# Optimization experiments

Measured on AMD Instinct MI355X. Metric: run time of the kernel, lower is better.

## Reference

```python
import jax, jax.numpy as jnp
import numpy as np

T, N, F, E, P, G, H, B = 8, 40000, 256, 640000, 128, 128, 128, 1024

def setup_inputs() -> dict:
    key = jax.random.key(0)
    ks = jax.random.split(key, 20)
    s = 0.05
    inp = {
        "x": jax.random.normal(ks[0], (T, N, F), jnp.float32),
        "edge_index": jax.random.randint(ks[1], (2, E), 0, N, dtype=jnp.int64),
        "target_indices": jax.random.randint(ks[2], (B,), 0, N, dtype=jnp.int64),
        # projection layer
        "proj_w": jax.random.normal(ks[3], (F, P), jnp.float32) * s,
        "proj_b": jnp.zeros((P,), jnp.float32),
        # GCN layers (weight + bias, symmetric-norm GCNConv with self-loops)
        "gcn_w1": jax.random.normal(ks[4], (P, G), jnp.float32) * s,
        "gcn_b1": jnp.zeros((G,), jnp.float32),
        "gcn_w2": jax.random.normal(ks[5], (G, G), jnp.float32) * s,
        "gcn_b2": jnp.zeros((G,), jnp.float32),
        # GRU (PyTorch layout: [3H, in], gates order r,z,n)
        "gru_w_ih": jax.random.normal(ks[6], (3 * H, 2 * G), jnp.float32) * s,
        "gru_w_hh": jax.random.normal(ks[7], (3 * H, H), jnp.float32) * s,
        "gru_b_ih": jnp.zeros((3 * H,), jnp.float32),
        "gru_b_hh": jnp.zeros((3 * H,), jnp.float32),
        # attention pooling
        "attn_w": jax.random.normal(ks[8], (H, 1), jnp.float32) * s,
        "attn_b": jnp.zeros((1,), jnp.float32),
        # predictor MLP (dropout in eval mode -> identity)
        "pred_w1": jax.random.normal(ks[9], (H, 16), jnp.float32) * s,
        "pred_b1": jnp.zeros((16,), jnp.float32),
        "pred_w2": jax.random.normal(ks[10], (16, 1), jnp.float32) * s,
        "pred_b2": jnp.zeros((1,), jnp.float32),
    }
    return inp


def reference(x, edge_index, target_indices, proj_w, proj_b, gcn_w1, gcn_b1,
              gcn_w2, gcn_b2, gru_w_ih, gru_w_hh, gru_b_ih, gru_b_hh,
              attn_w, attn_b, pred_w1, pred_b1, pred_w2, pred_b2):
    n = x.shape[1]
    # GCNConv normalization: add self-loops, deg^-1/2 A_hat deg^-1/2
    loops = jnp.arange(n, dtype=edge_index.dtype)
    src = jnp.concatenate([edge_index[0], loops])
    dst = jnp.concatenate([edge_index[1], loops])
    deg = jax.ops.segment_sum(jnp.ones_like(src, x.dtype), dst, num_segments=n)
    dinv = jnp.where(deg > 0, jax.lax.rsqrt(deg), 0.0)
    norm = (dinv[src] * dinv[dst])[:, None]  # [E+N, 1]

    def gcn_layer(h, w, b):
        m = h @ w                               # [N, G]
        agg = jax.ops.segment_sum(m[src] * norm, dst, num_segments=n)
        return jax.nn.relu(agg + b)

    def per_step(xt):
        h = jax.nn.relu(xt @ proj_w + proj_b)    # projection
        h1 = gcn_layer(h, gcn_w1, gcn_b1)
        h2 = gcn_layer(h1, gcn_w2, gcn_b2)
        return jnp.concatenate([h1, h2], axis=-1)  # jumping-knowledge concat

    emb = jax.vmap(per_step)(x)                  # [T, N, 2G]
    tgt = emb[:, target_indices]                 # [T, B, 2G]

    hdim = gru_w_hh.shape[1]
    def gru_cell(h, xt):
        gi = xt @ gru_w_ih.T + gru_b_ih
        gh = h @ gru_w_hh.T + gru_b_hh
        ir, iz, ig = jnp.split(gi, 3, axis=-1)
        hr, hz, hg = jnp.split(gh, 3, axis=-1)
        r = jax.nn.sigmoid(ir + hr)
        z = jax.nn.sigmoid(iz + hz)
        g = jnp.tanh(ig + r * hg)
        h_new = (1.0 - z) * g + z * h
        return h_new, h_new

    h0 = jnp.zeros((tgt.shape[1], hdim), x.dtype)
    _, outs = jax.lax.scan(gru_cell, h0, tgt)    # [T, B, H]
    rnn_out = outs.transpose(1, 0, 2)            # [B, T, H]

    scores = jnp.tanh(rnn_out @ attn_w + attn_b)       # [B, T, 1]
    attn_weights = jax.nn.softmax(scores, axis=1)
    rep = jnp.sum(rnn_out * attn_weights, axis=1)      # [B, H]

    hmid = jax.nn.relu(rep @ pred_w1 + pred_b1)        # dropout: eval mode
    pred = hmid @ pred_w2 + pred_b2                    # [B, 1]
    return pred, attn_weights.squeeze(-1)
```

## Files before the change

### kernel.cpp

```cpp
#include <hip/hip_runtime.h>
#include <stdint.h>

#define TT 8
#define NN 40000
#define FF 256
#define EE 640000
#define BB 1024
#define ROWS 320000

typedef __attribute__((ext_vector_type(8))) short s16x8;
typedef __attribute__((ext_vector_type(4))) float f32x4;

__device__ __forceinline__ unsigned short f2bf(float f){
  unsigned int u = __float_as_uint(f);
  u += 0x7fffu + ((u >> 16) & 1u);
  return (unsigned short)(u >> 16);
}
__device__ __forceinline__ float bflo(unsigned int u){ return __uint_as_float(u << 16); }
__device__ __forceinline__ float bfhi(unsigned int u){ return __uint_as_float(u & 0xffff0000u); }

__device__ __forceinline__ void gl2lds16(const void* g, void* l){
  auto gp = reinterpret_cast<const unsigned int __attribute__((address_space(1)))*>(
      reinterpret_cast<uintptr_t>(g));
  auto lp = reinterpret_cast<unsigned int __attribute__((address_space(3)))*>(
      static_cast<unsigned int>(reinterpret_cast<uintptr_t>(l)));
  __builtin_amdgcn_global_load_lds(gp, lp, 16, 0, 0);
}

__global__ void prep_k(const float* __restrict__ proj_w, const float* __restrict__ w1,
                       const float* __restrict__ w2, const float* __restrict__ wih,
                       const float* __restrict__ whh,
                       unsigned short* __restrict__ projwt, unsigned short* __restrict__ w1t,
                       unsigned short* __restrict__ w2t, unsigned short* __restrict__ wihb,
                       uint2* __restrict__ whhp)
{
  int i = blockIdx.x * 256 + threadIdx.x;
  if (i < 32768) {
    int p = i >> 8, f = i & 255;
    projwt[i] = f2bf(proj_w[f * 128 + p]);
  } else if (i < 49152) {
    int k = i - 32768; int o = k >> 7, c = k & 127;
    w1t[k] = f2bf(w1[c * 128 + o]);
  } else if (i < 65536) {
    int k = i - 49152; int o = k >> 7, c = k & 127;
    w2t[k] = f2bf(w2[c * 128 + o]);
  } else if (i < 163840) {
    int k = i - 65536;
    wihb[k] = f2bf(wih[k]);
  } else if (i < 180224) {
    int k = i - 163840; int kk = k >> 7, j = k & 127;
    unsigned int lo = (unsigned int)f2bf(whh[j * 128 + kk]) |
                      ((unsigned int)f2bf(whh[(128 + j) * 128 + kk]) << 16);
    unsigned int hi = (unsigned int)f2bf(whh[(256 + j) * 128 + kk]);
    whhp[k] = make_uint2(lo, hi);
  }
}

__global__ void init_k(int* __restrict__ counts, int* __restrict__ fill){
  int i = blockIdx.x * 256 + threadIdx.x;
  if (i < NN) { counts[i] = 0; fill[i] = 0; }
}
__global__ void count_k(const int* __restrict__ dst, int* __restrict__ counts){
  int i = blockIdx.x * 256 + threadIdx.x;
  if (i < EE) atomicAdd(&counts[dst[i]], 1);
}
__global__ void scan_k(const int* __restrict__ counts, int* __restrict__ rp,
                       float* __restrict__ dinv)
{
  __shared__ int sums[1024];
  const int CH = 40;
  int t = threadIdx.x;
  int beg = t * CH, end = beg + CH; if (end > NN) end = NN; if (beg > NN) beg = NN;
  int s = 0;
  for (int i = beg; i < end; i++) s += counts[i];
  sums[t] = s;
  __syncthreads();
  for (int off = 1; off < 1024; off <<= 1) {
    int add = (t >= off) ? sums[t - off] : 0;
    __syncthreads();
    sums[t] += add;
    __syncthreads();
  }
  int run = sums[t] - s;
  for (int i = beg; i < end; i++) { rp[i] = run; run += counts[i]; }
  if (t == 1023) rp[NN] = sums[1023];
  for (int i = beg; i < end; i++) dinv[i] = rsqrtf((float)(counts[i] + 1));
}
__global__ void fill_k(const int* __restrict__ src, const int* __restrict__ dst,
                       const int* __restrict__ rp, int* __restrict__ fill,
                       int* __restrict__ ci)
{
  int i = blockIdx.x * 256 + threadIdx.x;
  if (i < EE) {
    int d = dst[i];
    int pos = rp[d] + atomicAdd(&fill[d], 1);
    ci[pos] = src[i];
  }
}

template<int AF32, int MODE>
__global__ __launch_bounds__(256)
void gemm_k(const void* __restrict__ Ap, const short* __restrict__ Bt,
            void* __restrict__ Cp, int K, int ldc,
            const float* __restrict__ bias, const float* __restrict__ dinv)
{
  __shared__ short lA[128 * 64];
  __shared__ short lB[128 * 64];
  const int tid = threadIdx.x;
  const int lane = tid & 63, wave = tid >> 6;
  const int row0 = blockIdx.x * 128;
  const int col0 = blockIdx.y * 128;
  const int qr = (wave & 1) * 64, qc = (wave >> 1) * 64;
  const int m = lane & 15, q = lane >> 4;

  f32x4 acc[4][4];
#pragma unroll
  for (int i = 0; i < 4; i++)
#pragma unroll
    for (int j = 0; j < 4; j++) acc[i][j] = (f32x4){0.f, 0.f, 0.f, 0.f};

  for (int k0 = 0; k0 < K; k0 += 64) {
    __syncthreads();
    if (AF32) {
      const float* A = (const float*)Ap;
      int row = tid >> 1, half = tid & 1;
      const float* gp = A + (size_t)(row0 + row) * K + k0 + half * 32;
#pragma unroll
      for (int gi = 0; gi < 4; gi++) {
        float4 v0 = *(const float4*)(gp + gi * 8);
        float4 v1 = *(const float4*)(gp + gi * 8 + 4);
        uint4 w;
        w.x = (unsigned)f2bf(v0.x) | ((unsigned)f2bf(v0.y) << 16);
        w.y = (unsigned)f2bf(v0.z) | ((unsigned)f2bf(v0.w) << 16);
        w.z = (unsigned)f2bf(v1.x) | ((unsigned)f2bf(v1.y) << 16);
        w.w = (unsigned)f2bf(v1.z) | ((unsigned)f2bf(v1.w) << 16);
        int g = half * 4 + gi;
        *(uint4*)&lA[row * 64 + ((g ^ (row & 7)) * 8)] = w;
      }
    } else {
      const short* A = (const short*)Ap;
#pragma unroll
      for (int i = 0; i < 4; i++) {
        int c = wave * 4 + i;
        int row = c * 8 + (lane >> 3);
        int kg = (lane & 7) ^ (row & 7);
        gl2lds16(A + (size_t)(row0 + row) * K + k0 + kg * 8, lA + c * 512);
      }
    }
#pragma unroll
    for (int i = 0; i < 4; i++) {
      int c = wave * 4 + i;
      int row = c * 8 + (lane >> 3);
      int kg = (lane & 7) ^ (row & 7);
      gl2lds16(Bt + (size_t)(col0 + row) * K + k0 + kg * 8, lB + c * 512);
    }
    __syncthreads();
#pragma unroll
    for (int ks = 0; ks < 2; ks++) {
      s16x8 af[4], bf[4];
#pragma unroll
      for (int i = 0; i < 4; i++) {
        int R = qr + 16 * i + m;
        af[i] = *(const s16x8*)&lA[R * 64 + (((ks * 4 + q) ^ (R & 7)) * 8)];
        int RB = qc + 16 * i + m;
        bf[i] = *(const s16x8*)&lB[RB * 64 + (((ks * 4 + q) ^ (RB & 7)) * 8)];
      }
#pragma unroll
      for (int i = 0; i < 4; i++)
#pragma unroll
        for (int j = 0; j < 4; j++)
          acc[i][j] = __builtin_amdgcn_mfma_f32_16x16x32_bf16(af[i], bf[j], acc[i][j], 0, 0, 0);
    }
  }
#pragma unroll
  for (int i = 0; i < 4; i++) {
    int rbase = row0 + qr + 16 * i + q * 4;
#pragma unroll
    for (int j = 0; j < 4; j++) {
      int col = col0 + qc + 16 * j + m;
#pragma unroll
      for (int rr = 0; rr < 4; rr++) {
        int rg = rbase + rr;
        float v = acc[i][j][rr];
        if (MODE == 0) {
          v += bias[col]; v = fmaxf(v, 0.f);
          ((unsigned short*)Cp)[(size_t)rg * ldc + col] = f2bf(v);
        } else if (MODE == 1) {
          v *= dinv[rg % NN];
          ((unsigned short*)Cp)[(size_t)rg * ldc + col] = f2bf(v);
        } else {
          ((float*)Cp)[(size_t)rg * ldc + col] = v;
        }
      }
    }
  }
}

__global__ __launch_bounds__(256)
void agg_k(const unsigned int* __restrict__ Ms, unsigned int* __restrict__ Hout,
           const int* __restrict__ rp, const int* __restrict__ ci,
           const float* __restrict__ dinv, const float* __restrict__ bias)
{
  int widx = blockIdx.x * 4 + (threadIdx.x >> 6);
  int lane = threadIdx.x & 63;
  int t = widx / NN;
  int v = widx - t * NN;
  const unsigned int* base = Ms + (size_t)t * NN * 64 + lane;

  unsigned int su = base[(size_t)v * 64];
  float a0 = bflo(su), a1 = bfhi(su);

  int e0 = rp[v], e1 = rp[v + 1];
  for (int chunk = e0; chunk < e1; chunk += 64) {
    int cnt = min(64, e1 - chunk);
    int myIdx = (lane < cnt) ? ci[chunk + lane] : 0;
    int j = 0;
    for (; j + 4 <= cnt; j += 4) {
      int s0 = __shfl(myIdx, j, 64);
      int s1 = __shfl(myIdx, j + 1, 64);
      int s2 = __shfl(myIdx, j + 2, 64);
      int s3 = __shfl(myIdx, j + 3, 64);
      unsigned int w0 = base[(size_t)s0 * 64];
      unsigned int w1 = base[(size_t)s1 * 64];
      unsigned int w2 = base[(size_t)s2 * 64];
      unsigned int w3 = base[(size_t)s3 * 64];
      a0 += bflo(w0) + bflo(w1) + bflo(w2) + bflo(w3);
      a1 += bfhi(w0) + bfhi(w1) + bfhi(w2) + bfhi(w3);
    }
    for (; j < cnt; j++) {
      int s = __shfl(myIdx, j, 64);
      unsigned int w = base[(size_t)s * 64];
      a0 += bflo(w); a1 += bfhi(w);
    }
  }
  float dv = dinv[v];
  float b0 = bias[lane * 2], b1 = bias[lane * 2 + 1];
  float r0 = fmaxf(fmaf(dv, a0, b0), 0.f);
  float r1 = fmaxf(fmaf(dv, a1, b1), 0.f);
  Hout[(size_t)widx * 64 + lane] = (unsigned int)f2bf(r0) | ((unsigned int)f2bf(r1) << 16);
}

__global__ void gather_k(const unsigned int* __restrict__ h1, const unsigned int* __restrict__ h2,
                         const int* __restrict__ tix, unsigned int* __restrict__ TGT)
{
  int i = blockIdx.x * 256 + threadIdx.x;
  int dw = i & 127; int r = i >> 7; int b = r & 1023; int t = r >> 10;
  int node = tix[b];
  size_t src = ((size_t)t * NN + node) * 64 + (dw & 63);
  unsigned int val = (dw < 64) ? h1[src] : h2[src];
  TGT[(size_t)r * 128 + dw] = val;
}

__global__ __launch_bounds__(256)
void gru_attn_k(const float* __restrict__ GI, const uint2* __restrict__ Whp,
                const float* __restrict__ b_ih, const float* __restrict__ b_hh,
                const float* __restrict__ attw, const float* __restrict__ attb,
                float* __restrict__ rep, float* __restrict__ out_attn)
{
  __shared__ float hbuf[2][128];
  __shared__ float red[2][2];
  __shared__ float sc[2][8];
  int tid = threadIdx.x;
  int r = tid >> 7, j = tid & 127;
  int lane = tid & 63, wv = tid >> 6;
  int b = blockIdx.x * 2 + r;
  hbuf[r][j] = 0.f;
  float bi0 = b_ih[j], bi1 = b_ih[128 + j], bi2 = b_ih[256 + j];
  float bh0 = b_hh[j], bh1 = b_hh[128 + j], bh2 = b_hh[256 + j];
  float aw = attw[j], ab = attb[0];
  float ht[8];
  __syncthreads();
  for (int t = 0; t < 8; t++) {
    const float* gi = GI + ((size_t)(t * 1024 + b)) * 384;
    float accr = bh0, accz = bh1, accg = bh2;
#pragma unroll 4
    for (int k = 0; k < 128; k++) {
      float hk = hbuf[r][k];
      uint2 wp = Whp[k * 128 + j];
      accr += hk * bflo(wp.x);
      accz += hk * bfhi(wp.x);
      accg += hk * bflo(wp.y);
    }
    float x0 = gi[j] + bi0, x1 = gi[128 + j] + bi1, x2 = gi[256 + j] + bi2;
    float rg = 1.f / (1.f + __expf(-(x0 + accr)));
    float z  = 1.f / (1.f + __expf(-(x1 + accz)));
    float g  = tanhf(x2 + rg * accg);
    float hp = hbuf[r][j];
    float hn = (1.f - z) * g + z * hp;
    __syncthreads();
    hbuf[r][j] = hn;
    float p = hn * aw;
    for (int off = 32; off; off >>= 1) p += __shfl_down(p, off, 64);
    if (lane == 0) red[wv >> 1][wv & 1] = p;
    __syncthreads();
    if (j == 0) sc[r][t] = tanhf(red[r][0] + red[r][1] + ab);
    ht[t] = hn;
  }
  __syncthreads();
  float s[8], mx = -1e30f;
#pragma unroll
  for (int t = 0; t < 8; t++) { s[t] = sc[r][t]; mx = fmaxf(mx, s[t]); }
  float sum = 0.f;
#pragma unroll
  for (int t = 0; t < 8; t++) { s[t] = __expf(s[t] - mx); sum += s[t]; }
  float inv = 1.f / sum;
  float rv = 0.f;
#pragma unroll
  for (int t = 0; t < 8; t++) rv += s[t] * inv * ht[t];
  rep[(size_t)b * 128 + j] = rv;
  if (j < 8) out_attn[b * 8 + j] = s[j] * inv;
}

__global__ void pred_k(const float* __restrict__ rep, const float* __restrict__ w1,
                       const float* __restrict__ b1, const float* __restrict__ w2,
                       const float* __restrict__ b2, float* __restrict__ out)
{
  int bidx = blockIdx.x * 256 + threadIdx.x;
  if (bidx >= 1024) return;
  const float* rp = rep + (size_t)bidx * 128;
  float acc[16];
#pragma unroll
  for (int i = 0; i < 16; i++) acc[i] = b1[i];
  for (int k = 0; k < 128; k++) {
    float rv = rp[k];
#pragma unroll
    for (int i = 0; i < 16; i++) acc[i] += rv * w1[k * 16 + i];
  }
  float pv = b2[0];
#pragma unroll
  for (int i = 0; i < 16; i++) pv += fmaxf(acc[i], 0.f) * w2[i];
  out[bidx] = pv;
}

extern "C" void kernel_launch(void* const* d_in, const int* in_sizes, int n_in,
                              void* d_out, int out_size, void* d_ws, size_t ws_size,
                              hipStream_t stream)
{
  (void)in_sizes; (void)n_in; (void)out_size; (void)ws_size;
  const float* x      = (const float*)d_in[0];
  const int*   ei     = (const int*)d_in[1];
  const int*   tix    = (const int*)d_in[2];
  const float* proj_w = (const float*)d_in[3];
  const float* proj_b = (const float*)d_in[4];
  const float* gcn_w1 = (const float*)d_in[5];
  const float* gcn_b1 = (const float*)d_in[6];
  const float* gcn_w2 = (const float*)d_in[7];
  const float* gcn_b2 = (const float*)d_in[8];
  const float* w_ih   = (const float*)d_in[9];
  const float* w_hh   = (const float*)d_in[10];
  const float* b_ih   = (const float*)d_in[11];
  const float* b_hh   = (const float*)d_in[12];
  const float* attw   = (const float*)d_in[13];
  const float* attb   = (const float*)d_in[14];
  const float* pw1    = (const float*)d_in[15];
  const float* pb1    = (const float*)d_in[16];
  const float* pw2    = (const float*)d_in[17];
  const float* pb2    = (const float*)d_in[18];
  float* out = (float*)d_out;

  char* ws = (char*)d_ws;
  size_t off = 0;
  auto alloc = [&](size_t bytes) -> char* {
    char* p = ws + off; off += (bytes + 255) & ~(size_t)255; return p;
  };
  int*   counts = (int*)alloc((size_t)NN * 4);
  int*   fill   = (int*)alloc((size_t)NN * 4);
  int*   rp     = (int*)alloc((size_t)(NN + 1) * 4);
  float* dinv   = (float*)alloc((size_t)NN * 4);
  int*   ci     = (int*)alloc((size_t)EE * 4);
  unsigned short* projwt = (unsigned short*)alloc(128 * 256 * 2);
  unsigned short* w1t    = (unsigned short*)alloc(128 * 128 * 2);
  unsigned short* w2t    = (unsigned short*)alloc(128 * 128 * 2);
  unsigned short* wihb   = (unsigned short*)alloc(384 * 256 * 2);
  uint2* whhp            = (uint2*)alloc(128 * 128 * 8);
  unsigned int* TGT = (unsigned int*)alloc((size_t)8192 * 256 * 2);
  float* GI  = (float*)alloc((size_t)8192 * 384 * 4);
  float* rep = (float*)alloc((size_t)1024 * 128 * 4);
  unsigned short* bufA = (unsigned short*)alloc((size_t)ROWS * 128 * 2);
  unsigned short* bufB = (unsigned short*)alloc((size_t)ROWS * 128 * 2);
  unsigned short* bufC = (unsigned short*)alloc((size_t)ROWS * 128 * 2);

  const int* e_src = ei;
  const int* e_dst = ei + EE;

  prep_k<<<704, 256, 0, stream>>>(proj_w, gcn_w1, gcn_w2, w_ih, w_hh,
                                  projwt, w1t, w2t, wihb, whhp);
  init_k<<<157, 256, 0, stream>>>(counts, fill);
  count_k<<<2500, 256, 0, stream>>>(e_dst, counts);
  scan_k<<<1, 1024, 0, stream>>>(counts, rp, dinv);
  fill_k<<<2500, 256, 0, stream>>>(e_src, e_dst, rp, fill, ci);

  gemm_k<1, 0><<<dim3(2500, 1), 256, 0, stream>>>(x, (const short*)projwt, bufA,
                                                  256, 128, proj_b, nullptr);
  gemm_k<0, 1><<<dim3(2500, 1), 256, 0, stream>>>(bufA, (const short*)w1t, bufB,
                                                  128, 128, nullptr, dinv);
  agg_k<<<80000, 256, 0, stream>>>((const unsigned int*)bufB, (unsigned int*)bufC,
                                   rp, ci, dinv, gcn_b1);
  gemm_k<0, 1><<<dim3(2500, 1), 256, 0, stream>>>(bufC, (const short*)w2t, bufB,
                                                  128, 128, nullptr, dinv);
  agg_k<<<80000, 256, 0, stream>>>((const unsigned int*)bufB, (unsigned int*)bufA,
                                   rp, ci, dinv, gcn_b2);
  gather_k<<<4096, 256, 0, stream>>>((const unsigned int*)bufC, (const unsigned int*)bufA,
                                     tix, TGT);
  gemm_k<0, 2><<<dim3(64, 3), 256, 0, stream>>>(TGT, (const short*)wihb, GI,
                                                256, 384, nullptr, nullptr);
  gru_attn_k<<<512, 256, 0, stream>>>(GI, whhp, b_ih, b_hh, attw, attb, rep, out + 1024);
  pred_k<<<4, 256, 0, stream>>>(rep, pw1, pb1, pw2, pb2, out);
}
```

Baseline: 1.162 ms.

## Fuse projection and first GCN GEMM; split aggregation wave into two edge halves

```diff
diff --git a/kernel.cpp b/kernel.cpp
--- a/kernel.cpp
+++ b/kernel.cpp
@@ -98,11 +98,11 @@
   }
 }
 
-template<int AF32, int MODE>
+template<int MODE>
 __global__ __launch_bounds__(256)
 void gemm_k(const void* __restrict__ Ap, const short* __restrict__ Bt,
             void* __restrict__ Cp, int K, int ldc,
-            const float* __restrict__ bias, const float* __restrict__ dinv)
+            const float* __restrict__ dinv)
 {
   __shared__ short lA[128 * 64];
   __shared__ short lB[128 * 64];
@@ -121,10 +121,88 @@
 
   for (int k0 = 0; k0 < K; k0 += 64) {
     __syncthreads();
-    if (AF32) {
-      const float* A = (const float*)Ap;
+    {
+      const short* A = (const short*)Ap;
+#pragma unroll
+      for (int i = 0; i < 4; i++) {
+        int c = wave * 4 + i;
+        int row = c * 8 + (lane >> 3);
+        int kg = (lane & 7) ^ (row & 7);
+        gl2lds16(A + (size_t)(row0 + row) * K + k0 + kg * 8, lA + c * 512);
+      }
+    }
+#pragma unroll
+    for (int i = 0; i < 4; i++) {
+      int c = wave * 4 + i;
+      int row = c * 8 + (lane >> 3);
+      int kg = (lane & 7) ^ (row & 7);
+      gl2lds16(Bt + (size_t)(col0 + row) * K + k0 + kg * 8, lB + c * 512);
+    }
+    __syncthreads();
+#pragma unroll
+    for (int ks = 0; ks < 2; ks++) {
+      s16x8 af[4], bf[4];
+#pragma unroll
+      for (int i = 0; i < 4; i++) {
+        int R = qr + 16 * i + m;
+        af[i] = *(const s16x8*)&lA[R * 64 + (((ks * 4 + q) ^ (R & 7)) * 8)];
+        int RB = qc + 16 * i + m;
+        bf[i] = *(const s16x8*)&lB[RB * 64 + (((ks * 4 + q) ^ (RB & 7)) * 8)];
+      }
+#pragma unroll
+      for (int i = 0; i < 4; i++)
+#pragma unroll
+        for (int j = 0; j < 4; j++)
+          acc[i][j] = __builtin_amdgcn_mfma_f32_16x16x32_bf16(af[i], bf[j], acc[i][j], 0, 0, 0);
+    }
+  }
+#pragma unroll
+  for (int i = 0; i < 4; i++) {
+    int rbase = row0 + qr + 16 * i + q * 4;
+#pragma unroll
+    for (int j = 0; j < 4; j++) {
+      int col = col0 + qc + 16 * j + m;
+#pragma unroll
+      for (int rr = 0; rr < 4; rr++) {
+        int rg = rbase + rr;
+        float v = acc[i][j][rr];
+        if (MODE == 1) {
+          v *= dinv[rg % NN];
+          ((unsigned short*)Cp)[(size_t)rg * ldc + col] = f2bf(v);
+        } else {
+          ((float*)Cp)[(size_t)rg * ldc + col] = v;
+        }
+      }
+    }
+  }
+}
+
+__global__ __launch_bounds__(256)
+void projgcn_k(const float* __restrict__ x, const short* __restrict__ projwt,
+               const short* __restrict__ w1t, const float* __restrict__ proj_b,
+               const float* __restrict__ dinv, unsigned short* __restrict__ Ms1)
+{
+  __shared__ short lds[128 * 64 * 3];
+  short* lA = lds;
+  short* lB = lds + 8192;
+  short* lH = lds + 8192;
+  const int tid = threadIdx.x;
+  const int lane = tid & 63, wave = tid >> 6;
+  const int row0 = blockIdx.x * 128;
+  const int qr = (wave & 1) * 64, qc = (wave >> 1) * 64;
+  const int m = lane & 15, q = lane >> 4;
+
+  f32x4 acc[4][4];
+#pragma unroll
+  for (int i = 0; i < 4; i++)
+#pragma unroll
+    for (int j = 0; j < 4; j++) acc[i][j] = (f32x4){0.f, 0.f, 0.f, 0.f};
+
+  for (int k0 = 0; k0 < 256; k0 += 64) {
+    __syncthreads();
+    {
       int row = tid >> 1, half = tid & 1;
-      const float* gp = A + (size_t)(row0 + row) * K + k0 + half * 32;
+      const float* gp = x + (size_t)(row0 + row) * 256 + k0 + half * 32;
 #pragma unroll
       for (int gi = 0; gi < 4; gi++) {
         float4 v0 = *(const float4*)(gp + gi * 8);
@@ -137,22 +215,13 @@
         int g = half * 4 + gi;
         *(uint4*)&lA[row * 64 + ((g ^ (row & 7)) * 8)] = w;
       }
-    } else {
-      const short* A = (const short*)Ap;
-#pragma unroll
-      for (int i = 0; i < 4; i++) {
-        int c = wave * 4 + i;
-        int row = c * 8 + (lane >> 3);
-        int kg = (lane & 7) ^ (row & 7);
-        gl2lds16(A + (size_t)(row0 + row) * K + k0 + kg * 8, lA + c * 512);
-      }
     }
 #pragma unroll
     for (int i = 0; i < 4; i++) {
       int c = wave * 4 + i;
       int row = c * 8 + (lane >> 3);
       int kg = (lane & 7) ^ (row & 7);
-      gl2lds16(Bt + (size_t)(col0 + row) * K + k0 + kg * 8, lB + c * 512);
+      gl2lds16(projwt + (size_t)row * 256 + k0 + kg * 8, lB + c * 512);
     }
     __syncthreads();
 #pragma unroll
@@ -172,72 +241,135 @@
           acc[i][j] = __builtin_amdgcn_mfma_f32_16x16x32_bf16(af[i], bf[j], acc[i][j], 0, 0, 0);
     }
   }
+  __syncthreads();
+
+#pragma unroll
+  for (int i = 0; i < 4; i++) {
+    int rb = qr + 16 * i + q * 4;
+#pragma unroll
+    for (int j = 0; j < 4; j++) {
+      int c = qc + 16 * j + m;
+      int chalf = c & 64;
+      int gsw = (c >> 3) & 7;
+      float bv = proj_b[c];
+#pragma unroll
+      for (int rr = 0; rr < 4; rr++) {
+        int r_loc = rb + rr;
+        float v = fmaxf(acc[i][j][rr] + bv, 0.f);
+        lH[r_loc * 128 + chalf + ((gsw ^ (r_loc & 7)) << 3) + (c & 7)] = (short)f2bf(v);
+      }
+      acc[i][j] = (f32x4){0.f, 0.f, 0.f, 0.f};
+    }
+  }
+
+  for (int k0 = 0; k0 < 128; k0 += 64) {
+    __syncthreads();
+#pragma unroll
+    for (int i = 0; i < 4; i++) {
+      int c = wave * 4 + i;
+      int row = c * 8 + (lane >> 3);
+      int kg = (lane & 7) ^ (row & 7);
+      gl2lds16(w1t + (size_t)row * 128 + k0 + kg * 8, lA + c * 512);
+    }
+    __syncthreads();
+#pragma unroll
+    for (int ks = 0; ks < 2; ks++) {
+      s16x8 af[4], bf[4];
+#pragma unroll
+      for (int i = 0; i < 4; i++) {
+        int R = qr + 16 * i + m;
+        af[i] = *(const s16x8*)&lH[R * 128 + k0 + (((ks * 4 + q) ^ (R & 7)) << 3)];
+        int RB = qc + 16 * i + m;
+        bf[i] = *(const s16x8*)&lA[RB * 64 + (((ks * 4 + q) ^ (RB & 7)) << 3)];
+      }
+#pragma unroll
+      for (int i = 0; i < 4; i++)
+#pragma unroll
+        for (int j = 0; j < 4; j++)
+          acc[i][j] = __builtin_amdgcn_mfma_f32_16x16x32_bf16(af[i], bf[j], acc[i][j], 0, 0, 0);
+    }
+  }
+
 #pragma unroll
   for (int i = 0; i < 4; i++) {
     int rbase = row0 + qr + 16 * i + q * 4;
 #pragma unroll
     for (int j = 0; j < 4; j++) {
-      int col = col0 + qc + 16 * j + m;
+      int col = qc + 16 * j + m;
 #pragma unroll
       for (int rr = 0; rr < 4; rr++) {
         int rg = rbase + rr;
-        float v = acc[i][j][rr];
-        if (MODE == 0) {
-          v += bias[col]; v = fmaxf(v, 0.f);
-          ((unsigned short*)Cp)[(size_t)rg * ldc + col] = f2bf(v);
-        } else if (MODE == 1) {
-          v *= dinv[rg % NN];
-          ((unsigned short*)Cp)[(size_t)rg * ldc + col] = f2bf(v);
-        } else {
-          ((float*)Cp)[(size_t)rg * ldc + col] = v;
-        }
+        float v = acc[i][j][rr] * dinv[rg % NN];
+        Ms1[(size_t)rg * 128 + col] = f2bf(v);
       }
     }
   }
 }
 
 __global__ __launch_bounds__(256)
-void agg_k(const unsigned int* __restrict__ Ms, unsigned int* __restrict__ Hout,
+void agg_k(const uint2* __restrict__ Ms, uint2* __restrict__ Hout,
            const int* __restrict__ rp, const int* __restrict__ ci,
            const float* __restrict__ dinv, const float* __restrict__ bias)
 {
   int widx = blockIdx.x * 4 + (threadIdx.x >> 6);
   int lane = threadIdx.x & 63;
+  int li = lane & 31, h = lane >> 5;
   int t = widx / NN;
   int v = widx - t * NN;
-  const unsigned int* base = Ms + (size_t)t * NN * 64 + lane;
-
-  unsigned int su = base[(size_t)v * 64];
-  float a0 = bflo(su), a1 = bfhi(su);
+  const uint2* base = Ms + (size_t)t * NN * 32 + li;
+
+  uint2 su = base[(size_t)v * 32];
+  float a0, a1, a2, a3;
+  if (h == 0) { a0 = bflo(su.x); a1 = bfhi(su.x); a2 = bflo(su.y); a3 = bfhi(su.y); }
+  else        { a0 = 0.f; a1 = 0.f; a2 = 0.f; a3 = 0.f; }
 
   int e0 = rp[v], e1 = rp[v + 1];
   for (int chunk = e0; chunk < e1; chunk += 64) {
     int cnt = min(64, e1 - chunk);
     int myIdx = (lane < cnt) ? ci[chunk + lane] : 0;
     int j = 0;
-    for (; j + 4 <= cnt; j += 4) {
-      int s0 = __shfl(myIdx, j, 64);
-      int s1 = __shfl(myIdx, j + 1, 64);
-      int s2 = __shfl(myIdx, j + 2, 64);
-      int s3 = __shfl(myIdx, j + 3, 64);
-      unsigned int w0 = base[(size_t)s0 * 64];
-      unsigned int w1 = base[(size_t)s1 * 64];
-      unsigned int w2 = base[(size_t)s2 * 64];
-      unsigned int w3 = base[(size_t)s3 * 64];
-      a0 += bflo(w0) + bflo(w1) + bflo(w2) + bflo(w3);
-      a1 += bfhi(w0) + bfhi(w1) + bfhi(w2) + bfhi(w3);
-    }
-    for (; j < cnt; j++) {
+    for (; j + 8 <= cnt; j += 8) {
+      int s0 = __shfl(myIdx, j + h, 64);
+      int s1 = __shfl(myIdx, j + 2 + h, 64);
+      int s2 = __shfl(myIdx, j + 4 + h, 64);
+      int s3 = __shfl(myIdx, j + 6 + h, 64);
+      uint2 w0 = base[(size_t)s0 * 32];
+      uint2 w1 = base[(size_t)s1 * 32];
+      uint2 w2 = base[(size_t)s2 * 32];
+      uint2 w3 = base[(size_t)s3 * 32];
+      a0 += bflo(w0.x) + bflo(w1.x) + bflo(w2.x) + bflo(w3.x);
+      a1 += bfhi(w0.x) + bfhi(w1.x) + bfhi(w2.x) + bfhi(w3.x);
+      a2 += bflo(w0.y) + bflo(w1.y) + bflo(w2.y) + bflo(w3.y);
+      a3 += bfhi(w0.y) + bfhi(w1.y) + bfhi(w2.y) + bfhi(w3.y);
+    }
+    for (; j + 2 <= cnt; j += 2) {
+      int s = __shfl(myIdx, j + h, 64);
+      uint2 w = base[(size_t)s * 32];
+      a0 += bflo(w.x); a1 += bfhi(w.x); a2 += bflo(w.y); a3 += bfhi(w.y);
+    }
+    if (j < cnt) {
       int s = __shfl(myIdx, j, 64);
-      unsigned int w = base[(size_t)s * 64];
-      a0 += bflo(w); a1 += bfhi(w);
-    }
-  }
-  float dv = dinv[v];
-  float b0 = bias[lane * 2], b1 = bias[lane * 2 + 1];
-  float r0 = fmaxf(fmaf(dv, a0, b0), 0.f);
-  float r1 = fmaxf(fmaf(dv, a1, b1), 0.f);
-  Hout[(size_t)widx * 64 + lane] = (unsigned int)f2bf(r0) | ((unsigned int)f2bf(r1) << 16);
+      if (h == 0) {
+        uint2 w = base[(size_t)s * 32];
+        a0 += bflo(w.x); a1 += bfhi(w.x); a2 += bflo(w.y); a3 += bfhi(w.y);
+      }
+    }
+  }
+  a0 += __shfl_xor(a0, 32, 64);
+  a1 += __shfl_xor(a1, 32, 64);
+  a2 += __shfl_xor(a2, 32, 64);
+  a3 += __shfl_xor(a3, 32, 64);
+  if (h == 0) {
+    float dv = dinv[v];
+    float r0 = fmaxf(fmaf(dv, a0, bias[li * 4 + 0]), 0.f);
+    float r1 = fmaxf(fmaf(dv, a1, bias[li * 4 + 1]), 0.f);
+    float r2 = fmaxf(fmaf(dv, a2, bias[li * 4 + 2]), 0.f);
+    float r3 = fmaxf(fmaf(dv, a3, bias[li * 4 + 3]), 0.f);
+    uint2 o;
+    o.x = (unsigned)f2bf(r0) | ((unsigned)f2bf(r1) << 16);
+    o.y = (unsigned)f2bf(r2) | ((unsigned)f2bf(r3) << 16);
+    Hout[(size_t)widx * 32 + li] = o;
+  }
 }
 
 __global__ void gather_k(const unsigned int* __restrict__ h1, const unsigned int* __restrict__ h2,
@@ -390,20 +522,18 @@
   scan_k<<<1, 1024, 0, stream>>>(counts, rp, dinv);
   fill_k<<<2500, 256, 0, stream>>>(e_src, e_dst, rp, fill, ci);
 
-  gemm_k<1, 0><<<dim3(2500, 1), 256, 0, stream>>>(x, (const short*)projwt, bufA,
-                                                  256, 128, proj_b, nullptr);
-  gemm_k<0, 1><<<dim3(2500, 1), 256, 0, stream>>>(bufA, (const short*)w1t, bufB,
-                                                  128, 128, nullptr, dinv);
-  agg_k<<<80000, 256, 0, stream>>>((const unsigned int*)bufB, (unsigned int*)bufC,
+  projgcn_k<<<2500, 256, 0, stream>>>(x, (const short*)projwt, (const short*)w1t,
+                                      proj_b, dinv, bufB);
+  agg_k<<<80000, 256, 0, stream>>>((const uint2*)bufB, (uint2*)bufC,
                                    rp, ci, dinv, gcn_b1);
-  gemm_k<0, 1><<<dim3(2500, 1), 256, 0, stream>>>(bufC, (const short*)w2t, bufB,
-                                                  128, 128, nullptr, dinv);
-  agg_k<<<80000, 256, 0, stream>>>((const unsigned int*)bufB, (unsigned int*)bufA,
+  gemm_k<1><<<dim3(2500, 1), 256, 0, stream>>>(bufC, (const short*)w2t, bufB,
+                                               128, 128, dinv);
+  agg_k<<<80000, 256, 0, stream>>>((const uint2*)bufB, (uint2*)bufA,
                                    rp, ci, dinv, gcn_b2);
   gather_k<<<4096, 256, 0, stream>>>((const unsigned int*)bufC, (const unsigned int*)bufA,
                                      tix, TGT);
-  gemm_k<0, 2><<<dim3(64, 3), 256, 0, stream>>>(TGT, (const short*)wihb, GI,
-                                                256, 384, nullptr, nullptr);
+  gemm_k<2><<<dim3(64, 3), 256, 0, stream>>>(TGT, (const short*)wihb, GI,
+                                             256, 384, nullptr);
   gru_attn_k<<<512, 256, 0, stream>>>(GI, whhp, b_ih, b_hh, attw, attb, rep, out + 1024);
   pred_k<<<4, 256, 0, stream>>>(rep, pw1, pb1, pw2, pb2, out);
 }
```

Result: no change. 1.172 ms (+0.9%).
